# Kernel tuning notes

Hardware: AMD Instinct MI355X
Metric: run time of the kernel (lower is better)

Reference implementation:

```python
import jax, jax.numpy as jnp
import numpy as np

WINDOW = 16  # window_size from init_kwargs


def sigmoid_cutoff(x):
    # max(min(1.2*sigmoid(x) - 0.1, 1), 0)
    return jnp.clip(1.2 * jax.nn.sigmoid(x) - 0.1, 0.0, 1.0)


def setup_inputs() -> dict:
    key = jax.random.key(0)
    k1, k2, k3 = jax.random.split(key, 3)
    B, S, H = 8, 2048, 1024
    x = jax.random.normal(k1, (B, S, H), dtype=jnp.float32)
    # Dense kernels (glorot-ish scale), x_layer has no bias, y_layer has bias
    Wx = jax.random.normal(k2, (H, H), dtype=jnp.float32) * (1.0 / np.sqrt(H))
    Wy = jax.random.normal(k3, (H, 2 * H), dtype=jnp.float32) * (1.0 / np.sqrt(H))
    by = jnp.zeros((2 * H,), dtype=jnp.float32)
    return {"x": x, "Wx": Wx, "Wy": Wy, "by": by}


def reference(x, Wx, Wy, by):
    B, S, H = x.shape
    # left-pad sequence with window_size-1 zeros, then project once (x_layer)
    xp = jnp.pad(x, ((0, 0), (WINDOW - 1, 0), (0, 0)))
    proj = jnp.einsum('bsh,hd->bsd', xp, Wx)  # [B, S+W-1, H]

    def step(state, i):
        # inputs[:, i:S+i] in the original loop
        inp = jax.lax.dynamic_slice_in_dim(proj, i, S, axis=1)  # [B,S,H]
        ns = jnp.einsum('bsh,hd->bsd', state, Wy) + by          # [B,S,2H]
        # reshape [B,S,2,H]: channel 0 = candidate, channel 1 = gate
        cand, gate_logits = jnp.split(ns, 2, axis=-1)
        gate = sigmoid_cutoff(gate_logits)
        new_state = jax.nn.relu(gate * (inp + cand) + (1.0 - gate) * state)
        return new_state, None

    state0 = jnp.zeros_like(x)
    state, _ = jax.lax.scan(step, state0, jnp.arange(WINDOW))
    return state
```

## Files before the change

kernel.cpp:

```cpp
#include <hip/hip_runtime.h>

#define H 1024
#define SEQ 2048
#define MROWS 16384
#define KD 1024
#define NT32 32
#define EPW 72

typedef _Float16 f16;
typedef _Float16 f16x8 __attribute__((ext_vector_type(8)));
typedef float f32x4 __attribute__((ext_vector_type(4)));

__device__ __forceinline__ float gate_fn(float x) {
    float s = 1.0f / (1.0f + __expf(-x));
    return fminf(fmaxf(1.2f * s - 0.1f, 0.0f), 1.0f);
}

__device__ __forceinline__ size_t frag_off(int row, int k) {
    return ((size_t)((row >> 4) * 32 + (k >> 5))) * 512
         + (size_t)((((row & 15) | (((k >> 3) & 3) << 4)) << 3) + (k & 7));
}

__device__ __forceinline__ void gload_lds16(const void* g, void* lds) {
    __builtin_amdgcn_global_load_lds(
        (const __attribute__((address_space(1))) unsigned int*)g,
        (__attribute__((address_space(3))) unsigned int*)lds, 16, 0, 0);
}

__global__ void k_f32_to_f16(const float* __restrict__ in, f16* __restrict__ out) {
    size_t i = ((size_t)blockIdx.x * blockDim.x + threadIdx.x) * 8;
    float4 v0 = *(const float4*)(in + i);
    float4 v1 = *(const float4*)(in + i + 4);
    f16x8 o;
    o[0] = (f16)v0.x; o[1] = (f16)v0.y; o[2] = (f16)v0.z; o[3] = (f16)v0.w;
    o[4] = (f16)v1.x; o[5] = (f16)v1.y; o[6] = (f16)v1.z; o[7] = (f16)v1.w;
    *(f16x8*)(out + i) = o;
}

__global__ void k_transpose_f16(const float* __restrict__ Wsrc, f16* __restrict__ WT,
                                int K, int N) {
    __shared__ float tile[32][33];
    int n0 = blockIdx.x * 32, k0 = blockIdx.y * 32;
    for (int i = threadIdx.y; i < 32; i += 8)
        tile[i][threadIdx.x] = Wsrc[(size_t)(k0 + i) * N + n0 + threadIdx.x];
    __syncthreads();
    for (int i = threadIdx.y; i < 32; i += 8)
        WT[(size_t)(n0 + i) * K + k0 + threadIdx.x] = (f16)tile[threadIdx.x][i];
}

__global__ void k_transpose_fragB(const float* __restrict__ Wsrc, f16* __restrict__ WT) {
    __shared__ float tile[32][33];
    int n0 = blockIdx.x * 32, k0 = blockIdx.y * 32;
    for (int i = threadIdx.y; i < 32; i += 8)
        tile[i][threadIdx.x] = Wsrc[(size_t)(k0 + i) * (2 * H) + n0 + threadIdx.x];
    __syncthreads();
    int n = n0 + threadIdx.x;
#pragma unroll
    for (int r = 0; r < 4; ++r) {
        int i = threadIdx.y * 4 + r;
        int k = k0 + i;
        WT[frag_off(n, k)] = (f16)tile[i][threadIdx.x];
    }
}

__global__ __launch_bounds__(256) void k_proj_gemm(const f16* __restrict__ A,
                                                   const f16* __restrict__ BT,
                                                   f16* __restrict__ P16) {
    __shared__ alignas(16) f16 Alds[128 * 32];
    __shared__ alignas(16) f16 Blds[128 * 32];
    const int tid = threadIdx.x;
    const int lane = tid & 63, wid = tid >> 6;
    const int l15 = lane & 15, l4 = lane >> 4;
    const int bm = blockIdx.x, bn = blockIdx.y;

    const f16* gA[2]; const f16* gB[2];
    char* ldsA[2]; char* ldsB[2];
#pragma unroll
    for (int it = 0; it < 2; ++it) {
        int c = it * 4 + wid;
        int row = c * 16 + (lane >> 2);
        int kch = (lane & 3) ^ ((row >> 1) & 3);
        gA[it] = A + (size_t)(bm * 128 + row) * KD + kch * 8;
        gB[it] = BT + (size_t)(bn * 128 + row) * KD + kch * 8;
        ldsA[it] = (char*)Alds + c * 1024;
        ldsB[it] = (char*)Blds + c * 1024;
    }

    int offA[2], offB[8];
#pragma unroll
    for (int m = 0; m < 2; ++m) {
        int row = wid * 32 + m * 16 + l15;
        offA[m] = row * 64 + ((l4 ^ ((row >> 1) & 3)) << 4);
    }
#pragma unroll
    for (int n = 0; n < 8; ++n) {
        int row = n * 16 + l15;
        offB[n] = row * 64 + ((l4 ^ ((row >> 1) & 3)) << 4);
    }

    f32x4 acc[2][8] = {};

    for (int kt = 0; kt < KD / 32; ++kt) {
        __syncthreads();
#pragma unroll
        for (int it = 0; it < 2; ++it) {
            gload_lds16(gA[it], ldsA[it]);
            gload_lds16(gB[it], ldsB[it]);
            gA[it] += 32; gB[it] += 32;
        }
        __syncthreads();
        f16x8 a[2], b[8];
#pragma unroll
        for (int m = 0; m < 2; ++m) a[m] = *(const f16x8*)((const char*)Alds + offA[m]);
#pragma unroll
        for (int n = 0; n < 8; ++n) b[n] = *(const f16x8*)((const char*)Blds + offB[n]);
#pragma unroll
        for (int n = 0; n < 8; ++n)
#pragma unroll
            for (int m = 0; m < 2; ++m)
                acc[m][n] = __builtin_amdgcn_mfma_f32_16x16x32_f16(a[m], b[n], acc[m][n], 0, 0, 0);
    }

#pragma unroll
    for (int m = 0; m < 2; ++m)
#pragma unroll
        for (int n = 0; n < 8; ++n) {
            int col = bn * 128 + n * 16 + l15;
#pragma unroll
            for (int r = 0; r < 4; ++r) {
                int row = bm * 128 + wid * 32 + m * 16 + l4 * 4 + r;
                P16[(size_t)row * H + col] = (f16)acc[m][n][r];
            }
        }
}

__global__ void k_step0(const f16* __restrict__ P16, const float* __restrict__ by,
                        f16* __restrict__ S16) {
    size_t idx = ((size_t)blockIdx.x * blockDim.x + threadIdx.x) * 8;
    int row = (int)(idx >> 10);
    int d = (int)(idx & 1023);
    int s = row & (SEQ - 1);
    f16x8 p = {};
    if (s >= 15) p = *(const f16x8*)(P16 + (size_t)(row - 15) * H + d);
    float4 byc0 = *(const float4*)(by + d);
    float4 byc1 = *(const float4*)(by + d + 4);
    float4 byg0 = *(const float4*)(by + H + d);
    float4 byg1 = *(const float4*)(by + H + d + 4);
    f16x8 sv;
#pragma unroll
    for (int j = 0; j < 8; ++j) {
        float byc = (j < 4) ? ((const float*)&byc0)[j] : ((const float*)&byc1)[j - 4];
        float byg = (j < 4) ? ((const float*)&byg0)[j] : ((const float*)&byg1)[j - 4];
        float g = gate_fn(byg);
        float v = fmaxf(g * ((float)p[j] + byc), 0.f);
        sv[j] = (f16)v;
    }
    *(f16x8*)(S16 + frag_off(row, d)) = sv;
}

__global__ __launch_bounds__(512, 4) void k_step_gemm(const f16* __restrict__ A,
                                                      const f16* __restrict__ WyTF,
                                                      const f16* __restrict__ P16,
                                                      const float* __restrict__ by,
                                                      float* __restrict__ Out,
                                                      f16* __restrict__ Snext,
                                                      int stepi) {
    __shared__ alignas(16) char lds[73728];
    const int tid = threadIdx.x;
    const int lane = tid & 63, w = tid >> 6;
    const int l15 = lane & 15, l4 = lane >> 4;
    const int wr = w >> 1, wc = w & 1;

    const int orig = blockIdx.x;
    const int wg = (orig & 7) * 128 + (orig >> 3);
    const int bm = wg >> 4, tb = wg & 15;

    const char* ap[4];
#pragma unroll
    for (int m = 0; m < 4; ++m)
        ap[m] = (const char*)A + (size_t)(bm * 16 + wr * 4 + m) * 32768 + lane * 16;

    const char* bp[4];
#pragma unroll
    for (int n = 0; n < 4; ++n) {
        int brow16 = (n < 2) ? (tb * 4 + wc * 2 + n) : (64 + tb * 4 + wc * 2 + (n - 2));
        bp[n] = (const char*)WyTF + (size_t)brow16 * 32768 + lane * 16;
    }

    f32x4 acc[4][4] = {};

#pragma unroll 1
    for (int t = 0; t < NT32; ++t) {
        f16x8 a[4], b[4];
#pragma unroll
        for (int m = 0; m < 4; ++m) { a[m] = *(const f16x8*)ap[m]; ap[m] += 1024; }
#pragma unroll
        for (int n = 0; n < 4; ++n) { b[n] = *(const f16x8*)bp[n]; bp[n] += 1024; }
        __builtin_amdgcn_s_setprio(1);
#pragma unroll
        for (int m = 0; m < 4; ++m)
#pragma unroll
            for (int n = 0; n < 4; ++n)
                acc[m][n] = __builtin_amdgcn_mfma_f32_16x16x32_f16(a[m], b[n], acc[m][n], 0, 0, 0);
        __builtin_amdgcn_s_setprio(0);
    }

    const bool last = (stepi == 15);
    f16* Cand = (f16*)lds;
    f16* Gate = (f16*)(lds + 36864);
#pragma unroll
    for (int m = 0; m < 4; ++m)
#pragma unroll
        for (int n = 0; n < 2; ++n)
#pragma unroll
            for (int r4 = 0; r4 < 4; ++r4) {
                int row = wr * 64 + m * 16 + l4 * 4 + r4;
                int cc = wc * 32 + n * 16 + l15;
                Cand[row * EPW + cc] = (f16)acc[m][n][r4];
                Gate[row * EPW + cc] = (f16)acc[m][n + 2][r4];
            }
    __syncthreads();
    {
        const int g = tid & 7;
        const int rb = tid >> 3;
        const int dl = g * 8;
        const int d = tb * 64 + dl;
        float4 byc0 = *(const float4*)(by + d);
        float4 byc1 = *(const float4*)(by + d + 4);
        float4 byg0 = *(const float4*)(by + H + d);
        float4 byg1 = *(const float4*)(by + H + d + 4);
#pragma unroll
        for (int p = 0; p < 4; ++p) {
            int row = p * 64 + rb;
            int grow = bm * 256 + row;
            int s = grow & (SEQ - 1);
            size_t fa = frag_off(grow, d);
            f16x8 c8 = *(const f16x8*)(Cand + row * EPW + dl);
            f16x8 g8 = *(const f16x8*)(Gate + row * EPW + dl);
            f16x8 p8 = {};
            if (s >= 15 - stepi)
                p8 = *(const f16x8*)(P16 + (size_t)(grow + stepi - 15) * H + d);
            f16x8 s8 = *(const f16x8*)(A + fa);
            f16x8 o8; float ov[8];
#pragma unroll
            for (int j = 0; j < 8; ++j) {
                float byc = (j < 4) ? ((const float*)&byc0)[j] : ((const float*)&byc1)[j - 4];
                float byg = (j < 4) ? ((const float*)&byg0)[j] : ((const float*)&byg1)[j - 4];
                float cand = (float)c8[j] + byc;
                float gg = gate_fn((float)g8[j] + byg);
                float v = fmaxf(gg * ((float)p8[j] + cand) + (1.f - gg) * (float)s8[j], 0.f);
                o8[j] = (f16)v; ov[j] = v;
            }
            if (!last) {
                *(f16x8*)(Snext + fa) = o8;
            } else {
                *(float4*)(Out + (size_t)grow * H + d) = make_float4(ov[0], ov[1], ov[2], ov[3]);
                *(float4*)(Out + (size_t)grow * H + d + 4) = make_float4(ov[4], ov[5], ov[6], ov[7]);
            }
        }
    }
}

extern "C" void kernel_launch(void* const* d_in, const int* in_sizes, int n_in,
                              void* d_out, int out_size, void* d_ws, size_t ws_size,
                              hipStream_t stream) {
    (void)in_sizes; (void)n_in; (void)out_size; (void)ws_size;
    const float* x  = (const float*)d_in[0];
    const float* Wx = (const float*)d_in[1];
    const float* Wy = (const float*)d_in[2];
    const float* by = (const float*)d_in[3];
    float* out = (float*)d_out;

    char* ws = (char*)d_ws;
    const size_t MB = 1024ull * 1024ull;
    f16* st16a = (f16*)(ws);
    f16* st16b = (f16*)(ws + 32 * MB);
    f16* P16   = (f16*)(ws + 64 * MB);
    f16* WxT   = (f16*)(ws + 96 * MB);
    f16* WyTF  = (f16*)(ws + 98 * MB);

    hipLaunchKernelGGL(k_f32_to_f16, dim3(MROWS * H / 8 / 256), dim3(256), 0, stream, x, st16a);
    hipLaunchKernelGGL(k_transpose_f16, dim3(H / 32, H / 32), dim3(32, 8), 0, stream, Wx, WxT, H, H);
    hipLaunchKernelGGL(k_transpose_fragB, dim3(2 * H / 32, H / 32), dim3(32, 8), 0, stream, Wy, WyTF);
    hipLaunchKernelGGL(k_proj_gemm, dim3(MROWS / 128, H / 128), dim3(256), 0, stream, st16a, WxT, P16);
    hipLaunchKernelGGL(k_step0, dim3(MROWS * H / 8 / 256), dim3(256), 0, stream, P16, by, st16b);

    f16* bufs[2] = {st16a, st16b};
    for (int i = 1; i <= 15; ++i) {
        const f16* cur = bufs[i & 1];
        f16* nxt = bufs[(i + 1) & 1];
        hipLaunchKernelGGL(k_step_gemm, dim3(MROWS / 256 * 16), dim3(512), 0, stream,
                           cur, WyTF, P16, by, out, nxt, i);
    }
}
```

Measured before the change: 1.370 ms.

## Switch step GEMM to 32x32x16 MFMA with LDS-staged double-buffered weights

Changes the fragment layout of the state and transposed weights to 32-row blocks so the step GEMM can use 32x32x16 MFMA instructions instead of 16x16x32. Weight tiles are now shared across waves by loading them into double-buffered LDS via global_load_lds, while A fragments are still read directly from global memory. The aim is fewer redundant weight loads and higher MFMA efficiency, at the cost of a __syncthreads per K-iteration and a different epilogue mapping of accumulators to the candidate and gate LDS tiles.

```diff
diff --git a/kernel.cpp b/kernel.cpp
--- a/kernel.cpp
+++ b/kernel.cpp
@@ -10,15 +10,16 @@
 typedef _Float16 f16;
 typedef _Float16 f16x8 __attribute__((ext_vector_type(8)));
 typedef float f32x4 __attribute__((ext_vector_type(4)));
+typedef float f32x16 __attribute__((ext_vector_type(16)));
 
 __device__ __forceinline__ float gate_fn(float x) {
     float s = 1.0f / (1.0f + __expf(-x));
     return fminf(fmaxf(1.2f * s - 0.1f, 0.0f), 1.0f);
 }
 
-__device__ __forceinline__ size_t frag_off(int row, int k) {
-    return ((size_t)((row >> 4) * 32 + (k >> 5))) * 512
-         + (size_t)((((row & 15) | (((k >> 3) & 3) << 4)) << 3) + (k & 7));
+__device__ __forceinline__ size_t frag32_off(int row, int k) {
+    return ((size_t)((row >> 5) * 64 + (k >> 4))) * 512
+         + (size_t)((((row & 31) | (((k >> 3) & 1) << 5)) << 3) + (k & 7));
 }
 
 __device__ __forceinline__ void gload_lds16(const void* g, void* lds) {
@@ -59,7 +60,7 @@
     for (int r = 0; r < 4; ++r) {
         int i = threadIdx.y * 4 + r;
         int k = k0 + i;
-        WT[frag_off(n, k)] = (f16)tile[i][threadIdx.x];
+        WT[frag32_off(n, k)] = (f16)tile[i][threadIdx.x];
     }
 }
 
@@ -155,7 +156,7 @@
         float v = fmaxf(g * ((float)p[j] + byc), 0.f);
         sv[j] = (f16)v;
     }
-    *(f16x8*)(S16 + frag_off(row, d)) = sv;
+    *(f16x8*)(S16 + frag32_off(row, d)) = sv;
 }
 
 __global__ __launch_bounds__(512, 4) void k_step_gemm(const f16* __restrict__ A,
@@ -168,57 +169,75 @@
     __shared__ alignas(16) char lds[73728];
     const int tid = threadIdx.x;
     const int lane = tid & 63, w = tid >> 6;
-    const int l15 = lane & 15, l4 = lane >> 4;
     const int wr = w >> 1, wc = w & 1;
 
     const int orig = blockIdx.x;
     const int wg = (orig & 7) * 128 + (orig >> 3);
     const int bm = wg >> 4, tb = wg & 15;
 
-    const char* ap[4];
-#pragma unroll
-    for (int m = 0; m < 4; ++m)
-        ap[m] = (const char*)A + (size_t)(bm * 16 + wr * 4 + m) * 32768 + lane * 16;
-
-    const char* bp[4];
-#pragma unroll
-    for (int n = 0; n < 4; ++n) {
-        int brow16 = (n < 2) ? (tb * 4 + wc * 2 + n) : (64 + tb * 4 + wc * 2 + (n - 2));
-        bp[n] = (const char*)WyTF + (size_t)brow16 * 32768 + lane * 16;
-    }
-
-    f32x4 acc[4][4] = {};
+    const char* ap[2];
+#pragma unroll
+    for (int m = 0; m < 2; ++m)
+        ap[m] = (const char*)A + (size_t)(bm * 8 + wr * 2 + m) * 65536 + lane * 16;
+
+    const int nbS = w >> 1;
+    const int nrowS = (nbS < 2) ? (tb * 2 + nbS) : (32 + tb * 2 + (nbS - 2));
+    const char* pBsrc = (const char*)WyTF + (size_t)nrowS * 65536 + (size_t)(w & 1) * 1024 + lane * 16;
+#define STAGEB(bp) do { gload_lds16(pBsrc, (bp) + w * 1024 + lane * 16); pBsrc += 2048; } while (0)
+
+    const int offBc = (wc * 2) * 1024 + lane * 16;
+    const int offBg = ((2 + wc) * 2) * 1024 + lane * 16;
+
+    f32x16 accC[2] = {}, accG[2] = {};
+
+    char* cb = lds;
+    char* nx = lds + 8192;
+
+    STAGEB(cb);
+    __syncthreads();
 
 #pragma unroll 1
     for (int t = 0; t < NT32; ++t) {
-        f16x8 a[4], b[4];
-#pragma unroll
-        for (int m = 0; m < 4; ++m) { a[m] = *(const f16x8*)ap[m]; ap[m] += 1024; }
-#pragma unroll
-        for (int n = 0; n < 4; ++n) { b[n] = *(const f16x8*)bp[n]; bp[n] += 1024; }
+        f16x8 a0[2], a1[2];
+#pragma unroll
+        for (int m = 0; m < 2; ++m) {
+            a0[m] = *(const f16x8*)ap[m];
+            a1[m] = *(const f16x8*)(ap[m] + 1024);
+            ap[m] += 2048;
+        }
+        if (t + 1 < NT32) STAGEB(nx);
+        f16x8 bc0 = *(const f16x8*)(cb + offBc);
+        f16x8 bc1 = *(const f16x8*)(cb + offBc + 1024);
+        f16x8 bg0 = *(const f16x8*)(cb + offBg);
+        f16x8 bg1 = *(const f16x8*)(cb + offBg + 1024);
         __builtin_amdgcn_s_setprio(1);
 #pragma unroll
-        for (int m = 0; m < 4; ++m)
-#pragma unroll
-            for (int n = 0; n < 4; ++n)
-                acc[m][n] = __builtin_amdgcn_mfma_f32_16x16x32_f16(a[m], b[n], acc[m][n], 0, 0, 0);
+        for (int m = 0; m < 2; ++m) {
+            accC[m] = __builtin_amdgcn_mfma_f32_32x32x16_f16(a0[m], bc0, accC[m], 0, 0, 0);
+            accG[m] = __builtin_amdgcn_mfma_f32_32x32x16_f16(a0[m], bg0, accG[m], 0, 0, 0);
+            accC[m] = __builtin_amdgcn_mfma_f32_32x32x16_f16(a1[m], bc1, accC[m], 0, 0, 0);
+            accG[m] = __builtin_amdgcn_mfma_f32_32x32x16_f16(a1[m], bg1, accG[m], 0, 0, 0);
+        }
         __builtin_amdgcn_s_setprio(0);
-    }
+        __syncthreads();
+        char* tmp = cb; cb = nx; nx = tmp;
+    }
+#undef STAGEB
 
     const bool last = (stepi == 15);
     f16* Cand = (f16*)lds;
     f16* Gate = (f16*)(lds + 36864);
-#pragma unroll
-    for (int m = 0; m < 4; ++m)
-#pragma unroll
-        for (int n = 0; n < 2; ++n)
-#pragma unroll
-            for (int r4 = 0; r4 < 4; ++r4) {
-                int row = wr * 64 + m * 16 + l4 * 4 + r4;
-                int cc = wc * 32 + n * 16 + l15;
-                Cand[row * EPW + cc] = (f16)acc[m][n][r4];
-                Gate[row * EPW + cc] = (f16)acc[m][n + 2][r4];
-            }
+    const int crow0 = 4 * (lane >> 5);
+    const int ccol = lane & 31;
+#pragma unroll
+    for (int m = 0; m < 2; ++m)
+#pragma unroll
+        for (int r = 0; r < 16; ++r) {
+            int row = wr * 64 + m * 32 + (r & 3) + 8 * (r >> 2) + crow0;
+            int cc = wc * 32 + ccol;
+            Cand[row * EPW + cc] = (f16)accC[m][r];
+            Gate[row * EPW + cc] = (f16)accG[m][r];
+        }
     __syncthreads();
     {
         const int g = tid & 7;
@@ -234,7 +253,7 @@
             int row = p * 64 + rb;
             int grow = bm * 256 + row;
             int s = grow & (SEQ - 1);
-            size_t fa = frag_off(grow, d);
+            size_t fa = frag32_off(grow, d);
             f16x8 c8 = *(const f16x8*)(Cand + row * EPW + dl);
             f16x8 g8 = *(const f16x8*)(Gate + row * EPW + dl);
             f16x8 p8 = {};
```

Result: slower. 1.450 ms (+5.9%).
